# Optimization experiments

Measured on AMD Instinct MI355X. Metric: run time of the kernel, lower is better.

Reference implementation:

```python
import jax, jax.numpy as jnp
import numpy as np

EMBED_DIM = 1024
NUM_HEADS = 16
HEAD_DIM = EMBED_DIM // NUM_HEADS
SCALING = HEAD_DIM ** -0.5
TGT_LEN, BSZ = 2048, 2


def setup_inputs() -> dict:
    key = jax.random.key(0)
    k1, k2, k3 = jax.random.split(key, 3)
    return {
        "query": jax.random.normal(k1, (TGT_LEN, BSZ, EMBED_DIM), jnp.float32),
        "in_proj_weight": jax.random.normal(k2, (3 * EMBED_DIM, EMBED_DIM), jnp.float32) * (EMBED_DIM ** -0.5),
        "in_proj_bias": jnp.zeros((3 * EMBED_DIM,), jnp.float32),
        "out_w": jax.random.normal(k3, (EMBED_DIM, EMBED_DIM), jnp.float32) * (EMBED_DIM ** -0.5),
        "out_b": jnp.zeros((EMBED_DIM,), jnp.float32),
    }


def reference(query, in_proj_weight, in_proj_bias, out_w, out_b):
    tgt_len, bsz, embed_dim = query.shape
    # fused QKV projection (self-attention path: qkv_same)
    qkv = query @ in_proj_weight.T + in_proj_bias  # [T, B, 3E]
    q, k, v = jnp.split(qkv, 3, axis=-1)
    q = q * SCALING
    # [T, B, E] -> [B*H, T, hd]
    def to_heads(x):
        return x.reshape(tgt_len, bsz * NUM_HEADS, HEAD_DIM).transpose(1, 0, 2)
    q, k, v = to_heads(q), to_heads(k), to_heads(v)
    attn_weights = jnp.einsum('bqd,bkd->bqk', q, k)          # [B*H, T, T]
    attn_weights = jax.nn.softmax(attn_weights, axis=-1)
    attn = jnp.einsum('bqk,bkd->bqd', attn_weights, v)       # [B*H, T, hd]
    attn = attn.transpose(1, 0, 2).reshape(tgt_len, bsz, embed_dim)
    attn = attn @ out_w.T + out_b
    # averaged attention weights over heads (need_weights=True)
    avg_weights = attn_weights.reshape(bsz, NUM_HEADS, tgt_len, tgt_len).mean(axis=1)
    return attn, avg_weights
```

## Files before the change

### kernel.cpp

```cpp
#include <hip/hip_runtime.h>
#include <hip/hip_bf16.h>
#include <math.h>

#define T_LEN 2048
#define BSZ   2
#define EMB   1024
#define NH    16
#define HD    64
#define BHN   (BSZ*NH)
#define M1    (T_LEN*BSZ)
#define SCAL  0.125f
#define QSCALE (0.125f * 1.44269504088896f)

typedef __attribute__((ext_vector_type(8))) short bf16x8;
typedef __attribute__((ext_vector_type(4))) float f32x4;
typedef __attribute__((ext_vector_type(2))) unsigned int u32x2;

__device__ inline unsigned short f2bf(float x) {
    union { float f; unsigned u; } v; v.f = x;
    unsigned r = v.u + 0x7FFF + ((v.u >> 16) & 1);
    return (unsigned short)(r >> 16);
}

__device__ inline unsigned pack2bf(float a, float b) {
    union { __hip_bfloat162 h; unsigned u; } v;
    v.h = __float22bfloat162_rn(make_float2(a, b));
    return v.u;
}

__device__ inline float fexp2(float x) {
#if __has_builtin(__builtin_amdgcn_exp2f)
    return __builtin_amdgcn_exp2f(x);
#else
    return exp2f(x);
#endif
}

__device__ inline void async16(const unsigned short* g, unsigned short* l) {
    __builtin_amdgcn_global_load_lds(
        (const __attribute__((address_space(1))) void*)g,
        (__attribute__((address_space(3))) void*)l, 16, 0, 0);
}

__device__ inline void bar() {
    asm volatile("" ::: "memory");
    __builtin_amdgcn_s_barrier();
    asm volatile("" ::: "memory");
}

__device__ inline const unsigned short* swz(const unsigned short* base, int r, int c) {
    return base + (((r << 3) + (c ^ (r & 7))) << 3);
}
__device__ inline const unsigned short* swz16(const unsigned short* base, int r, int c) {
    return base + (((r << 4) + (c ^ (r & 7))) << 3);
}

__device__ inline void xchg(unsigned e, unsigned o, unsigned& w_lo, unsigned& w_hi) {
#if __has_builtin(__builtin_amdgcn_permlane32_swap) && __has_builtin(__builtin_amdgcn_permlane16_swap)
    u32x2 x = __builtin_amdgcn_permlane32_swap(e, o, false, false);
    u32x2 y = __builtin_amdgcn_permlane16_swap(x[0], x[1], false, false);
    w_lo = y[0]; w_hi = y[1];
#else
    int lane = (int)(threadIdx.x & 63);
    int quad = lane >> 4, l16 = lane & 15;
    int srcA = ((quad & 1) * 2) * 16 + l16;
    int srcB = ((quad & 1) * 2 + 1) * 16 + l16;
    unsigned ea = (unsigned)__shfl((int)e, srcA, 64);
    unsigned oa = (unsigned)__shfl((int)o, srcA, 64);
    unsigned eb = (unsigned)__shfl((int)e, srcB, 64);
    unsigned ob = (unsigned)__shfl((int)o, srcB, 64);
    w_lo = (quad >> 1) ? oa : ea;
    w_hi = (quad >> 1) ? ob : eb;
#endif
}

__global__ __launch_bounds__(256) void cvt3_kernel(
    const float* __restrict__ s0, const float* __restrict__ s1,
    const float* __restrict__ s2, unsigned short* __restrict__ dst,
    int n0, int n1)
{
    int idx = blockIdx.x * 256 + threadIdx.x;
    const float* src; int o;
    if (idx < n0)           { src = s0; o = idx; }
    else if (idx < n0 + n1) { src = s1; o = idx - n0; }
    else                    { src = s2; o = idx - n0 - n1; }
    float4 a = reinterpret_cast<const float4*>(src)[(size_t)o * 2];
    float4 c = reinterpret_cast<const float4*>(src)[(size_t)o * 2 + 1];
    unsigned w[4] = { pack2bf(a.x, a.y), pack2bf(a.z, a.w),
                      pack2bf(c.x, c.y), pack2bf(c.z, c.w) };
    reinterpret_cast<uint4*>(dst)[idx] = *reinterpret_cast<uint4*>(w);
}

__global__ __launch_bounds__(256) void qkv_mfma_kernel(
    const unsigned short* __restrict__ A, const unsigned short* __restrict__ B,
    const float* __restrict__ bias,
    unsigned short* __restrict__ Q16, unsigned short* __restrict__ K16,
    unsigned short* __restrict__ Vt16)
{
    constexpr int BM = 128, BN = 128, BK = 32, K = 1024;
    __shared__ unsigned short As[BM * BK];
    __shared__ unsigned short Bs[BN * BK];
    const int tid = threadIdx.x;
    const int lane = tid & 63, wave = tid >> 6;
    const int quad = lane >> 4, l16 = lane & 15;
    const int wr = wave >> 1, wc = wave & 1;
    const int m0 = blockIdx.x * BM, n0 = blockIdx.y * BN;

    f32x4 zero4 = {0.f, 0.f, 0.f, 0.f};
    f32x4 acc[4][4];
    #pragma unroll
    for (int i = 0; i < 4; ++i)
        #pragma unroll
        for (int j = 0; j < 4; ++j) acc[i][j] = zero4;

    for (int k0 = 0; k0 < K; k0 += BK) {
        __syncthreads();
        #pragma unroll
        for (int t = 0; t < 2; ++t) {
            int c = t * 256 + tid;
            int m = c >> 2, kb = c & 3;
            async16(&A[(size_t)(m0 + m) * K + k0 + kb * 8], &As[c * 8]);
            async16(&B[(size_t)(n0 + m) * K + k0 + kb * 8], &Bs[c * 8]);
        }
        __syncthreads();
        bf16x8 af[4], bfr[4];
        #pragma unroll
        for (int i = 0; i < 4; ++i) {
            af[i]  = *reinterpret_cast<const bf16x8*>(&As[(wr * 64 + i * 16 + l16) * BK + quad * 8]);
            bfr[i] = *reinterpret_cast<const bf16x8*>(&Bs[(wc * 64 + i * 16 + l16) * BK + quad * 8]);
        }
        #pragma unroll
        for (int i = 0; i < 4; ++i)
            #pragma unroll
            for (int j = 0; j < 4; ++j)
                acc[i][j] = __builtin_amdgcn_mfma_f32_16x16x32_bf16(af[i], bfr[j], acc[i][j], 0, 0, 0);
    }

    #pragma unroll
    for (int j = 0; j < 4; ++j) {
        int n = n0 + wc * 64 + j * 16 + l16;
        float bv = bias[n];
        int which = n >> 10;
        int c = n & 1023;
        int h = c >> 6, d = c & 63;
        #pragma unroll
        for (int i = 0; i < 4; ++i) {
            #pragma unroll
            for (int r = 0; r < 4; ++r) {
                int m = m0 + wr * 64 + i * 16 + quad * 4 + r;
                int t = m >> 1, b = m & 1;
                int bh = b * NH + h;
                float v = acc[i][j][r] + bv;
                if (which == 0)      Q16[((size_t)bh * T_LEN + t) * HD + d] = f2bf(v * QSCALE);
                else if (which == 1) K16[((size_t)bh * T_LEN + t) * HD + d] = f2bf(v);
                else                 Vt16[((size_t)bh * HD + d) * T_LEN + t] = f2bf(v);
            }
        }
    }
}

__global__ __launch_bounds__(512, 4) void flash_mfma_kernel(
    const unsigned short* __restrict__ Qb, const unsigned short* __restrict__ Kb,
    const unsigned short* __restrict__ Vt, unsigned short* __restrict__ AO,
    float* __restrict__ Rrow)
{
    __shared__ unsigned short Ks[2][128 * 64];
    __shared__ unsigned short Vs[2][64 * 128];
    const int tid = threadIdx.x;
    const int lane = tid & 63, wave = tid >> 6;
    const int quad = lane >> 4, l16 = lane & 15;

    const int lin = blockIdx.y * gridDim.x + blockIdx.x;
    const int xcd = lin & 7, slot = lin >> 3;
    const int bh = xcd * 4 + (slot >> 4);
    const int qt = slot & 15;
    const int q0 = qt * 128;
    const int b = bh >> 4, h = bh & 15;

    const unsigned short* Qp =
        Qb + ((size_t)bh * T_LEN + q0 + wave * 16 + l16) * HD;
    bf16x8 qf0 = *reinterpret_cast<const bf16x8*>(Qp + quad * 8);
    bf16x8 qf1 = *reinterpret_cast<const bf16x8*>(Qp + 32 + quad * 8);

    f32x4 zero4 = {0.f, 0.f, 0.f, 0.f};
    f32x4 oacc[4] = {zero4, zero4, zero4, zero4};
    float l_part = 0.f;

    const unsigned short* Kbase = Kb + (size_t)bh * T_LEN * HD;
    const unsigned short* Vbase = Vt + (size_t)bh * HD * T_LEN;

    const int ck0 = tid, ck1 = tid + 512;
    const int kr0 = ck0 >> 3, kc0 = (ck0 & 7) ^ (kr0 & 7);
    const int kr1 = ck1 >> 3, kc1 = (ck1 & 7) ^ (kr1 & 7);
    const int vr0 = ck0 >> 4, vc0 = (ck0 & 15) ^ (vr0 & 7);
    const int vr1 = ck1 >> 4, vc1 = (ck1 & 15) ^ (vr1 & 7);

    auto stage = [&](int buf, int kt) {
        async16(&Kbase[(size_t)(kt + kr0) * HD + kc0 * 8], &Ks[buf][ck0 * 8]);
        async16(&Kbase[(size_t)(kt + kr1) * HD + kc1 * 8], &Ks[buf][ck1 * 8]);
        async16(&Vbase[(size_t)vr0 * T_LEN + kt + vc0 * 8], &Vs[buf][ck0 * 8]);
        async16(&Vbase[(size_t)vr1 * T_LEN + kt + vc1 * 8], &Vs[buf][ck1 * 8]);
    };

    stage(0, 0);

    int cur = 0;
    for (int kt = 0; kt < T_LEN; kt += 128) {
        if (kt + 128 < T_LEN) {
            stage(cur ^ 1, kt + 128);
            asm volatile("s_waitcnt vmcnt(4)" ::: "memory");
        } else {
            asm volatile("s_waitcnt vmcnt(0)" ::: "memory");
        }
        bar();

        const unsigned short* Kt = Ks[cur];
        const unsigned short* Vv = Vs[cur];

        unsigned dlo[8], dhi[8];
        #pragma unroll
        for (int half = 0; half < 2; ++half) {
            f32x4 sacc[4] = {zero4, zero4, zero4, zero4};
            __builtin_amdgcn_s_setprio(1);
            #pragma unroll
            for (int j = 0; j < 4; ++j) {
                int kb = half * 4 + j;
                bf16x8 kf0 = *reinterpret_cast<const bf16x8*>(swz(Kt, kb * 16 + l16, quad));
                sacc[j] = __builtin_amdgcn_mfma_f32_16x16x32_bf16(kf0, qf0, sacc[j], 0, 0, 0);
                bf16x8 kf1 = *reinterpret_cast<const bf16x8*>(swz(Kt, kb * 16 + l16, 4 + quad));
                sacc[j] = __builtin_amdgcn_mfma_f32_16x16x32_bf16(kf1, qf1, sacc[j], 0, 0, 0);
            }
            __builtin_amdgcn_s_setprio(0);
            #pragma unroll
            for (int j = 0; j < 4; ++j) {
                float p0 = fexp2(sacc[j][0]);
                float p1 = fexp2(sacc[j][1]);
                float p2 = fexp2(sacc[j][2]);
                float p3 = fexp2(sacc[j][3]);
                l_part += (p0 + p1) + (p2 + p3);
                dlo[half * 4 + j] = pack2bf(p0, p1);
                dhi[half * 4 + j] = pack2bf(p2, p3);
            }
        }

        __builtin_amdgcn_s_setprio(1);
        #pragma unroll
        for (int ks = 0; ks < 4; ++ks) {
            unsigned w0, w1, w2, w3;
            xchg(dlo[2 * ks], dlo[2 * ks + 1], w0, w2);
            xchg(dhi[2 * ks], dhi[2 * ks + 1], w1, w3);
            union { bf16x8 v; unsigned u[4]; } P;
            P.u[0] = w0; P.u[1] = w1; P.u[2] = w2; P.u[3] = w3;
            #pragma unroll
            for (int dt = 0; dt < 4; ++dt) {
                bf16x8 va = *reinterpret_cast<const bf16x8*>(swz16(Vv, dt * 16 + l16, ks * 4 + quad));
                oacc[dt] = __builtin_amdgcn_mfma_f32_16x16x32_bf16(va, P.v, oacc[dt], 0, 0, 0);
            }
        }
        __builtin_amdgcn_s_setprio(0);

        bar();
        cur ^= 1;
    }

    l_part += __shfl_xor(l_part, 16);
    l_part += __shfl_xor(l_part, 32);
    float rl = 1.0f / l_part;
    int q = q0 + wave * 16 + l16;
    size_t base = ((size_t)q * BSZ + b) * EMB + h * HD;
    #pragma unroll
    for (int dt = 0; dt < 4; ++dt) {
        unsigned o[2] = { pack2bf(oacc[dt][0] * rl, oacc[dt][1] * rl),
                          pack2bf(oacc[dt][2] * rl, oacc[dt][3] * rl) };
        *reinterpret_cast<uint2*>(&AO[base + dt * 16 + quad * 4]) = *reinterpret_cast<uint2*>(o);
    }
    if (quad == 0)
        Rrow[(size_t)bh * T_LEN + q] = rl;
}

__global__ __launch_bounds__(512, 4) void avg_mfma_kernel(
    const unsigned short* __restrict__ Qb, const unsigned short* __restrict__ Kb,
    const float* __restrict__ Rrow, float* __restrict__ avg_out)
{
    __shared__ unsigned short Ks[2][2][128 * 64];
    const int tid = threadIdx.x;
    const int lane = tid & 63, wave = tid >> 6;
    const int quad = lane >> 4, l16 = lane & 15;
    const int kt = blockIdx.x, qt = blockIdx.y, b = blockIdx.z;
    const int q0 = qt * 128, k0 = kt * 128;

    auto stage_pair = [&](int buf, int h0) {
        const unsigned short* Kg = Kb + ((size_t)(b * NH + h0) * T_LEN + k0) * HD;
        #pragma unroll
        for (int t = 0; t < 4; ++t) {
            int c = t * 512 + tid;
            int hh = c >> 10, cl = c & 1023;
            int r = cl >> 3, cc = (cl & 7) ^ (r & 7);
            async16(&Kg[(size_t)hh * T_LEN * HD + (size_t)r * HD + cc * 8],
                    &Ks[buf][0][0] + (size_t)c * 8);
        }
    };

    f32x4 zero4 = {0.f, 0.f, 0.f, 0.f};
    f32x4 acc[8];
    #pragma unroll
    for (int kb = 0; kb < 8; ++kb) acc[kb] = zero4;

    stage_pair(0, 0);
    int cur = 0;
    for (int g = 0; g < NH / 2; ++g) {
        if (g + 1 < NH / 2) {
            stage_pair(cur ^ 1, 2 * (g + 1));
            asm volatile("s_waitcnt vmcnt(4)" ::: "memory");
        } else {
            asm volatile("s_waitcnt vmcnt(0)" ::: "memory");
        }
        bar();

        #pragma unroll
        for (int hh = 0; hh < 2; ++hh) {
            const int bh = b * NH + 2 * g + hh;
            const unsigned short* Kt = Ks[cur][hh];
            const int qrow = q0 + wave * 16;
            const unsigned short* Qp = Qb + ((size_t)bh * T_LEN + qrow + l16) * HD;
            bf16x8 qf0 = *reinterpret_cast<const bf16x8*>(Qp + quad * 8);
            bf16x8 qf1 = *reinterpret_cast<const bf16x8*>(Qp + 32 + quad * 8);
            float4 rlv = *reinterpret_cast<const float4*>(
                &Rrow[(size_t)bh * T_LEN + qrow + quad * 4]);

            f32x4 sacc[8];
            __builtin_amdgcn_s_setprio(1);
            #pragma unroll
            for (int kb = 0; kb < 8; ++kb) {
                sacc[kb] = zero4;
                bf16x8 kf0 = *reinterpret_cast<const bf16x8*>(swz(Kt, kb * 16 + l16, quad));
                sacc[kb] = __builtin_amdgcn_mfma_f32_16x16x32_bf16(qf0, kf0, sacc[kb], 0, 0, 0);
                bf16x8 kf1 = *reinterpret_cast<const bf16x8*>(swz(Kt, kb * 16 + l16, 4 + quad));
                sacc[kb] = __builtin_amdgcn_mfma_f32_16x16x32_bf16(qf1, kf1, sacc[kb], 0, 0, 0);
            }
            __builtin_amdgcn_s_setprio(0);

            float rl4[4] = { rlv.x, rlv.y, rlv.z, rlv.w };
            #pragma unroll
            for (int kb = 0; kb < 8; ++kb)
                #pragma unroll
                for (int r = 0; r < 4; ++r)
                    acc[kb][r] += fexp2(sacc[kb][r]) * rl4[r];
        }
        bar();
        cur ^= 1;
    }

    #pragma unroll
    for (int r = 0; r < 4; ++r) {
        int q = q0 + wave * 16 + quad * 4 + r;
        size_t base = ((size_t)b * T_LEN + q) * T_LEN + k0;
        #pragma unroll
        for (int kb = 0; kb < 8; ++kb)
            avg_out[base + kb * 16 + l16] = acc[kb][r] * (1.0f / 16.0f);
    }
}

__global__ __launch_bounds__(256) void out_mfma_kernel(
    const unsigned short* __restrict__ A, const unsigned short* __restrict__ B,
    const float* __restrict__ bias, float* __restrict__ out)
{
    constexpr int BM = 128, BN = 128, BK = 32, K = 1024;
    __shared__ unsigned short As[BM * BK];
    __shared__ unsigned short Bs[BN * BK];
    const int tid = threadIdx.x;
    const int lane = tid & 63, wave = tid >> 6;
    const int quad = lane >> 4, l16 = lane & 15;
    const int wr = wave >> 1, wc = wave & 1;
    const int m0 = blockIdx.x * BM, n0 = blockIdx.y * BN;

    f32x4 zero4 = {0.f, 0.f, 0.f, 0.f};
    f32x4 acc[4][4];
    #pragma unroll
    for (int i = 0; i < 4; ++i)
        #pragma unroll
        for (int j = 0; j < 4; ++j) acc[i][j] = zero4;

    for (int k0 = 0; k0 < K; k0 += BK) {
        __syncthreads();
        #pragma unroll
        for (int t = 0; t < 2; ++t) {
            int c = t * 256 + tid;
            int m = c >> 2, kb = c & 3;
            async16(&A[(size_t)(m0 + m) * K + k0 + kb * 8], &As[c * 8]);
            async16(&B[(size_t)(n0 + m) * K + k0 + kb * 8], &Bs[c * 8]);
        }
        __syncthreads();
        bf16x8 af[4], bfr[4];
        #pragma unroll
        for (int i = 0; i < 4; ++i) {
            af[i]  = *reinterpret_cast<const bf16x8*>(&As[(wr * 64 + i * 16 + l16) * BK + quad * 8]);
            bfr[i] = *reinterpret_cast<const bf16x8*>(&Bs[(wc * 64 + i * 16 + l16) * BK + quad * 8]);
        }
        #pragma unroll
        for (int i = 0; i < 4; ++i)
            #pragma unroll
            for (int j = 0; j < 4; ++j)
                acc[i][j] = __builtin_amdgcn_mfma_f32_16x16x32_bf16(af[i], bfr[j], acc[i][j], 0, 0, 0);
    }

    #pragma unroll
    for (int j = 0; j < 4; ++j) {
        int n = n0 + wc * 64 + j * 16 + l16;
        float bv = bias[n];
        #pragma unroll
        for (int i = 0; i < 4; ++i) {
            #pragma unroll
            for (int r = 0; r < 4; ++r) {
                int m = m0 + wr * 64 + i * 16 + quad * 4 + r;
                out[(size_t)m * 1024 + n] = acc[i][j][r] + bv;
            }
        }
    }
}

extern "C" void kernel_launch(void* const* d_in, const int* in_sizes, int n_in,
                              void* d_out, int out_size, void* d_ws, size_t ws_size,
                              hipStream_t stream)
{
    const float* query = (const float*)d_in[0];
    const float* wqkv  = (const float*)d_in[1];
    const float* bqkv  = (const float*)d_in[2];
    const float* wout  = (const float*)d_in[3];
    const float* bout  = (const float*)d_in[4];
    float* out = (float*)d_out;

    char* ws = (char*)d_ws;
    const size_t E_Q   = (size_t)M1 * EMB;
    const size_t E_W   = (size_t)3 * EMB * EMB;
    const size_t E_WO  = (size_t)EMB * EMB;
    const size_t E_QKV = (size_t)BHN * T_LEN * HD;

    unsigned short* queryb = (unsigned short*)ws;
    unsigned short* wqkvb  = queryb + E_Q;
    unsigned short* woutb  = wqkvb + E_W;
    unsigned short* Q16    = woutb + E_WO;
    unsigned short* K16    = Q16 + E_QKV;
    unsigned short* Vt16   = K16 + E_QKV;
    unsigned short* AO16   = Vt16 + E_QKV;
    float* Lr = (float*)(AO16 + E_Q);
    const size_t need = (E_Q + E_W + E_WO + 4 * E_QKV) * 2 + (size_t)BHN * T_LEN * 4;
    if (ws_size < need) return;

    cvt3_kernel<<<(int)((E_Q + E_W + E_WO) / 8 / 256), 256, 0, stream>>>(
        query, wqkv, wout, queryb, (int)(E_Q / 8), (int)(E_W / 8));

    qkv_mfma_kernel<<<dim3(M1 / 128, 3072 / 128), 256, 0, stream>>>(queryb, wqkvb, bqkv, Q16, K16, Vt16);
    flash_mfma_kernel<<<dim3(T_LEN / 128, BHN), 512, 0, stream>>>(Q16, K16, Vt16, AO16, Lr);
    avg_mfma_kernel<<<dim3(T_LEN / 128, T_LEN / 128, BSZ), 512, 0, stream>>>(Q16, K16, Lr, out + (size_t)M1 * EMB);
    out_mfma_kernel<<<dim3(M1 / 128, 1024 / 128), 256, 0, stream>>>(AO16, woutb, bout, out);
}
```

Measured before the change: 263.3 us.

## Retile head-averaged attention kernel to 64-key tiles with register-reused K fragments

Result: faster. 240.6 us (median of 2 runs) (-8.6%).

```diff
diff --git a/kernel.cpp b/kernel.cpp
--- a/kernel.cpp
+++ b/kernel.cpp
@@ -278,23 +278,23 @@
         Rrow[(size_t)bh * T_LEN + q] = rl;
 }
 
-__global__ __launch_bounds__(512, 4) void avg_mfma_kernel(
+__global__ __launch_bounds__(256) void avg_mfma_kernel(
     const unsigned short* __restrict__ Qb, const unsigned short* __restrict__ Kb,
     const float* __restrict__ Rrow, float* __restrict__ avg_out)
 {
-    __shared__ unsigned short Ks[2][2][128 * 64];
+    __shared__ unsigned short Ks[2][2][64 * 64];
     const int tid = threadIdx.x;
     const int lane = tid & 63, wave = tid >> 6;
     const int quad = lane >> 4, l16 = lane & 15;
     const int kt = blockIdx.x, qt = blockIdx.y, b = blockIdx.z;
-    const int q0 = qt * 128, k0 = kt * 128;
+    const int q0 = qt * 128, k0 = kt * 64;
 
     auto stage_pair = [&](int buf, int h0) {
         const unsigned short* Kg = Kb + ((size_t)(b * NH + h0) * T_LEN + k0) * HD;
         #pragma unroll
         for (int t = 0; t < 4; ++t) {
-            int c = t * 512 + tid;
-            int hh = c >> 10, cl = c & 1023;
+            int c = t * 256 + tid;
+            int hh = c >> 9, cl = c & 511;
             int r = cl >> 3, cc = (cl & 7) ^ (r & 7);
             async16(&Kg[(size_t)hh * T_LEN * HD + (size_t)r * HD + cc * 8],
                     &Ks[buf][0][0] + (size_t)c * 8);
@@ -302,9 +302,11 @@
     };
 
     f32x4 zero4 = {0.f, 0.f, 0.f, 0.f};
-    f32x4 acc[8];
-    #pragma unroll
-    for (int kb = 0; kb < 8; ++kb) acc[kb] = zero4;
+    f32x4 acc[2][4];
+    #pragma unroll
+    for (int s = 0; s < 2; ++s)
+        #pragma unroll
+        for (int c = 0; c < 4; ++c) acc[s][c] = zero4;
 
     stage_pair(0, 0);
     int cur = 0;
@@ -321,44 +323,52 @@
         for (int hh = 0; hh < 2; ++hh) {
             const int bh = b * NH + 2 * g + hh;
             const unsigned short* Kt = Ks[cur][hh];
-            const int qrow = q0 + wave * 16;
-            const unsigned short* Qp = Qb + ((size_t)bh * T_LEN + qrow + l16) * HD;
-            bf16x8 qf0 = *reinterpret_cast<const bf16x8*>(Qp + quad * 8);
-            bf16x8 qf1 = *reinterpret_cast<const bf16x8*>(Qp + 32 + quad * 8);
-            float4 rlv = *reinterpret_cast<const float4*>(
-                &Rrow[(size_t)bh * T_LEN + qrow + quad * 4]);
-
-            f32x4 sacc[8];
-            __builtin_amdgcn_s_setprio(1);
-            #pragma unroll
-            for (int kb = 0; kb < 8; ++kb) {
-                sacc[kb] = zero4;
-                bf16x8 kf0 = *reinterpret_cast<const bf16x8*>(swz(Kt, kb * 16 + l16, quad));
-                sacc[kb] = __builtin_amdgcn_mfma_f32_16x16x32_bf16(qf0, kf0, sacc[kb], 0, 0, 0);
-                bf16x8 kf1 = *reinterpret_cast<const bf16x8*>(swz(Kt, kb * 16 + l16, 4 + quad));
-                sacc[kb] = __builtin_amdgcn_mfma_f32_16x16x32_bf16(qf1, kf1, sacc[kb], 0, 0, 0);
-            }
-            __builtin_amdgcn_s_setprio(0);
-
-            float rl4[4] = { rlv.x, rlv.y, rlv.z, rlv.w };
-            #pragma unroll
-            for (int kb = 0; kb < 8; ++kb)
+            bf16x8 kf[4][2];
+            #pragma unroll
+            for (int c = 0; c < 4; ++c) {
+                kf[c][0] = *reinterpret_cast<const bf16x8*>(swz(Kt, c * 16 + l16, quad));
+                kf[c][1] = *reinterpret_cast<const bf16x8*>(swz(Kt, c * 16 + l16, 4 + quad));
+            }
+            #pragma unroll
+            for (int s = 0; s < 2; ++s) {
+                const int qrow = q0 + s * 64 + wave * 16;
+                const unsigned short* Qp = Qb + ((size_t)bh * T_LEN + qrow + l16) * HD;
+                bf16x8 qf0 = *reinterpret_cast<const bf16x8*>(Qp + quad * 8);
+                bf16x8 qf1 = *reinterpret_cast<const bf16x8*>(Qp + 32 + quad * 8);
+                float4 rlv = *reinterpret_cast<const float4*>(
+                    &Rrow[(size_t)bh * T_LEN + qrow + quad * 4]);
+
+                f32x4 sacc[4] = {zero4, zero4, zero4, zero4};
+                __builtin_amdgcn_s_setprio(1);
                 #pragma unroll
-                for (int r = 0; r < 4; ++r)
-                    acc[kb][r] += fexp2(sacc[kb][r]) * rl4[r];
+                for (int c = 0; c < 4; ++c) {
+                    sacc[c] = __builtin_amdgcn_mfma_f32_16x16x32_bf16(qf0, kf[c][0], sacc[c], 0, 0, 0);
+                    sacc[c] = __builtin_amdgcn_mfma_f32_16x16x32_bf16(qf1, kf[c][1], sacc[c], 0, 0, 0);
+                }
+                __builtin_amdgcn_s_setprio(0);
+
+                float rl4[4] = { rlv.x, rlv.y, rlv.z, rlv.w };
+                #pragma unroll
+                for (int c = 0; c < 4; ++c)
+                    #pragma unroll
+                    for (int r = 0; r < 4; ++r)
+                        acc[s][c][r] += fexp2(sacc[c][r]) * rl4[r];
+            }
         }
         bar();
         cur ^= 1;
     }
 
     #pragma unroll
-    for (int r = 0; r < 4; ++r) {
-        int q = q0 + wave * 16 + quad * 4 + r;
-        size_t base = ((size_t)b * T_LEN + q) * T_LEN + k0;
-        #pragma unroll
-        for (int kb = 0; kb < 8; ++kb)
-            avg_out[base + kb * 16 + l16] = acc[kb][r] * (1.0f / 16.0f);
-    }
+    for (int s = 0; s < 2; ++s)
+        #pragma unroll
+        for (int r = 0; r < 4; ++r) {
+            int q = q0 + s * 64 + wave * 16 + quad * 4 + r;
+            size_t base = ((size_t)b * T_LEN + q) * T_LEN + k0;
+            #pragma unroll
+            for (int c = 0; c < 4; ++c)
+                avg_out[base + c * 16 + l16] = acc[s][c][r] * (1.0f / 16.0f);
+        }
 }
 
 __global__ __launch_bounds__(256) void out_mfma_kernel(
@@ -452,6 +462,6 @@
 
     qkv_mfma_kernel<<<dim3(M1 / 128, 3072 / 128), 256, 0, stream>>>(queryb, wqkvb, bqkv, Q16, K16, Vt16);
     flash_mfma_kernel<<<dim3(T_LEN / 128, BHN), 512, 0, stream>>>(Q16, K16, Vt16, AO16, Lr);
-    avg_mfma_kernel<<<dim3(T_LEN / 128, T_LEN / 128, BSZ), 512, 0, stream>>>(Q16, K16, Lr, out + (size_t)M1 * EMB);
+    avg_mfma_kernel<<<dim3(T_LEN / 64, T_LEN / 128, BSZ), 256, 0, stream>>>(Q16, K16, Lr, out + (size_t)M1 * EMB);
     out_mfma_kernel<<<dim3(M1 / 128, 1024 / 128), 256, 0, stream>>>(AO16, woutb, bout, out);
 }
```
